# Kernel tuning notes

Measured on AMD Instinct MI355X. Metric: run time of the kernel, lower is better.

The kernel has to match this reference:

```python
import jax, jax.numpy as jnp
import numpy as np

N_NODES = 100000
N_EDGES = 1600000
N_GRAPHS = 64
D_IN, D_HID, D_OUT = 256, 128, 64
EPS = 1e-5


def gcn_conv(x, edge_index, edge_weight, W, b):
    """PyG GCNConv: add_self_loops=True, normalize=True (sym deg norm), bias."""
    n = x.shape[0]
    row = jnp.concatenate([edge_index[0], jnp.arange(n)])      # source
    col = jnp.concatenate([edge_index[1], jnp.arange(n)])      # target
    w = jnp.concatenate([edge_weight, jnp.ones((n,), x.dtype)])
    deg = jax.ops.segment_sum(w, col, num_segments=n)
    dinv = jnp.where(deg > 0, jax.lax.rsqrt(jnp.maximum(deg, EPS)), 0.0)
    norm = dinv[row] * w * dinv[col]                           # [E+N]
    h = x @ W                                                  # [N, out]
    msg = h[row] * norm[:, None]                               # [E+N, out]
    out = jax.ops.segment_sum(msg, col, num_segments=n)
    return out + b


def layer_norm(x, gamma, beta):
    mu = jnp.mean(x, axis=-1, keepdims=True)
    var = jnp.mean(jnp.square(x - mu), axis=-1, keepdims=True)
    return (x - mu) * jax.lax.rsqrt(var + EPS) * gamma + beta


def setup_inputs() -> dict:
    key = jax.random.key(0)
    ks = jax.random.split(key, 12)
    x = jax.random.normal(ks[0], (N_NODES, D_IN), jnp.float32)
    edge_index = jax.random.randint(ks[1], (2, N_EDGES), 0, N_NODES, jnp.int32)
    edge_weight = jax.random.uniform(ks[2], (N_EDGES,), jnp.float32)
    batch = jnp.sort(jax.random.randint(ks[3], (N_NODES,), 0, N_GRAPHS, jnp.int32))
    s1 = 1.0 / np.sqrt(D_IN)
    s2 = 1.0 / np.sqrt(D_HID)
    return {
        "x": x, "edge_index": edge_index, "edge_weight": edge_weight, "batch": batch,
        "W1": jax.random.uniform(ks[4], (D_IN, D_HID), jnp.float32, -s1, s1),
        "b1": jnp.zeros((D_HID,), jnp.float32),
        "g1": jnp.ones((D_HID,), jnp.float32),
        "bt1": jnp.zeros((D_HID,), jnp.float32),
        "W2": jax.random.uniform(ks[5], (D_HID, D_OUT), jnp.float32, -s2, s2),
        "b2": jnp.zeros((D_OUT,), jnp.float32),
        "g2": jnp.ones((D_OUT,), jnp.float32),
        "bt2": jnp.zeros((D_OUT,), jnp.float32),
    }


def reference(x, edge_index, edge_weight, batch, W1, b1, g1, bt1, W2, b2, g2, bt2):
    # ConvLayer 1: GCNConv -> relu -> LayerNorm(node)
    h = gcn_conv(x, edge_index, edge_weight, W1, b1)
    h = layer_norm(jax.nn.relu(h), g1, bt1)
    # dropout is identity in eval mode
    # ConvLayer 2
    h = gcn_conv(h, edge_index, edge_weight, W2, b2)
    h = layer_norm(jax.nn.relu(h), g2, bt2)
    # global mean pool over batch vector
    sums = jax.ops.segment_sum(h, batch, num_segments=N_GRAPHS)
    cnts = jax.ops.segment_sum(jnp.ones((h.shape[0],), h.dtype), batch, num_segments=N_GRAPHS)
    pooled = sums / jnp.maximum(cnts, 1.0)[:, None]
    return jax.nn.sigmoid(pooled)
```

## Files before the change

kernel.cpp:

```cpp
#include <hip/hip_runtime.h>
#include <cstdint>

#define EPSV 1e-5f

typedef __bf16 bf16x8 __attribute__((ext_vector_type(8)));
typedef __bf16 bf16x2 __attribute__((ext_vector_type(2)));
typedef float  f32x4  __attribute__((ext_vector_type(4)));
typedef unsigned long long u64;

__device__ __forceinline__ unsigned char f32_to_fp8(float x) {
    const int p = __builtin_amdgcn_cvt_pk_fp8_f32(x, x, 0, false);
    return (unsigned char)(p & 0xFF);
}

__global__ __launch_bounds__(256) void k_scanA(const u64* __restrict__ dc,
                                               float* __restrict__ dinv,
                                               int* __restrict__ cnt,
                                               int* __restrict__ bsum, int N) {
    __shared__ int ws[4];
    const int i = blockIdx.x * 256 + threadIdx.x;
    int v = 0;
    if (i < N) {
        const u64 p = dc[i];
        v = (int)(p >> 40);
        const float deg = 1.0f + (float)(p & 0xFFFFFFFFFFull) * (1.0f / 16777216.0f);
        dinv[i] = rsqrtf(deg);
        cnt[i] = v;
    }
#pragma unroll
    for (int o = 32; o >= 1; o >>= 1) v += __shfl_xor(v, o);
    if ((threadIdx.x & 63) == 0) ws[threadIdx.x >> 6] = v;
    __syncthreads();
    if (threadIdx.x == 0) bsum[blockIdx.x] = ws[0] + ws[1] + ws[2] + ws[3];
}

__global__ __launch_bounds__(256) void k_scan2(int* __restrict__ bsum, int NB) {
    __shared__ int carry;
    __shared__ int wsum[4];
    if (threadIdx.x == 0) carry = 0;
    __syncthreads();
    const int lane = threadIdx.x & 63, w = threadIdx.x >> 6;
    for (int base = 0; base < NB; base += 256) {
        const int i = base + threadIdx.x;
        const int v = (i < NB) ? bsum[i] : 0;
        int s = v;
#pragma unroll
        for (int o = 1; o < 64; o <<= 1) {
            const int t = __shfl_up(s, o);
            if (lane >= o) s += t;
        }
        if (lane == 63) wsum[w] = s;
        __syncthreads();
        int add = carry;
        for (int k = 0; k < w; ++k) add += wsum[k];
        const int tot = wsum[0] + wsum[1] + wsum[2] + wsum[3];
        if (i < NB) bsum[i] = add + s - v;
        __syncthreads();
        if (threadIdx.x == 0) carry += tot;
        __syncthreads();
    }
}

__global__ __launch_bounds__(256) void k_scan3(const int* __restrict__ cnt,
                                               const int* __restrict__ bsum,
                                               int* __restrict__ off, int N) {
    __shared__ int wsum[4];
    const int i = blockIdx.x * 256 + threadIdx.x;
    const int v = (i < N) ? cnt[i] : 0;
    const int lane = threadIdx.x & 63, w = threadIdx.x >> 6;
    int s = v;
#pragma unroll
    for (int o = 1; o < 64; o <<= 1) {
        const int t = __shfl_up(s, o);
        if (lane >= o) s += t;
    }
    if (lane == 63) wsum[w] = s;
    __syncthreads();
    int add = bsum[blockIdx.x];
    for (int k = 0; k < w; ++k) add += wsum[k];
    if (i < N) off[i] = add + s - v;
}

__global__ __launch_bounds__(256) void k_fill(const int* __restrict__ ei,
                                              const float* __restrict__ ew,
                                              const float* __restrict__ dinv,
                                              const int* __restrict__ off,
                                              const unsigned short* __restrict__ rank,
                                              float2* __restrict__ ern, int E) {
    const int e = blockIdx.x * 256 + threadIdx.x;
    if (e >= E) return;
    const int r = ei[e];
    const int c = ei[E + e];
    const int p = off[c] + (int)rank[e];
    ern[p] = make_float2(__int_as_float(r), dinv[r] * ew[e] * dinv[c]);
}

__global__ __launch_bounds__(256) void k_wcvt(const float* __restrict__ W1,
                                              __bf16* __restrict__ Wt1,
                                              const float* __restrict__ W2,
                                              __bf16* __restrict__ Wt2) {
    const int idx = blockIdx.x * 256 + threadIdx.x;
    if (idx < 256 * 128) {
        const int k = idx >> 7, c = idx & 127;
        Wt1[(((k >> 3) << 7) + c) * 8 + (k & 7)] = (__bf16)W1[idx];
    } else if (idx < 256 * 128 + 128 * 64) {
        const int j = idx - 256 * 128;
        const int k = j >> 6, c = j & 63;
        Wt2[(((k >> 3) << 6) + c) * 8 + (k & 7)] = (__bf16)W2[j];
    }
}

template <int K, int NOUT, bool ABF16>
__device__ __forceinline__ void mm_body(int bid, int tid, const void* __restrict__ Xv,
                                        const __bf16* __restrict__ WtB,
                                        unsigned char* __restrict__ H, int N) {
    constexpr int NCB = NOUT / 16;
    constexpr int NKB = K / 32;
    const int w = tid >> 6, l = tid & 63;
    const int r0 = l & 15, kq = l >> 4;
    const long tb0 = (long)bid * 128 + w * 32;
    const long ar0 = (tb0 + r0) < N ? (tb0 + r0) : (long)N - 1;
    const long ar1 = (tb0 + 16 + r0) < N ? (tb0 + 16 + r0) : (long)N - 1;

    f32x4 acc[2][NCB];
#pragma unroll
    for (int rf = 0; rf < 2; ++rf)
#pragma unroll
        for (int cb = 0; cb < NCB; ++cb) acc[rf][cb] = (f32x4){0.f, 0.f, 0.f, 0.f};

#define LDA(kb, a0, a1)                                                          \
    {                                                                            \
        const int koff = (kb) * 32 + kq * 8;                                     \
        if constexpr (ABF16) {                                                   \
            a0 = *reinterpret_cast<const bf16x8*>((const __bf16*)Xv + ar0 * K + koff); \
            a1 = *reinterpret_cast<const bf16x8*>((const __bf16*)Xv + ar1 * K + koff); \
        } else {                                                                 \
            const float* p0 = (const float*)Xv + ar0 * K + koff;                 \
            const float* p1 = (const float*)Xv + ar1 * K + koff;                 \
            const float4 u0 = *reinterpret_cast<const float4*>(p0);              \
            const float4 u1 = *reinterpret_cast<const float4*>(p0 + 4);          \
            const float4 u2 = *reinterpret_cast<const float4*>(p1);              \
            const float4 u3 = *reinterpret_cast<const float4*>(p1 + 4);          \
            a0[0] = (__bf16)u0.x; a0[1] = (__bf16)u0.y; a0[2] = (__bf16)u0.z;    \
            a0[3] = (__bf16)u0.w; a0[4] = (__bf16)u1.x; a0[5] = (__bf16)u1.y;    \
            a0[6] = (__bf16)u1.z; a0[7] = (__bf16)u1.w;                          \
            a1[0] = (__bf16)u2.x; a1[1] = (__bf16)u2.y; a1[2] = (__bf16)u2.z;    \
            a1[3] = (__bf16)u2.w; a1[4] = (__bf16)u3.x; a1[5] = (__bf16)u3.y;    \
            a1[6] = (__bf16)u3.z; a1[7] = (__bf16)u3.w;                          \
        }                                                                        \
    }

#define LDB(kb, b)                                                               \
    {                                                                            \
        const __bf16* bp = WtB + (long)(((kb) * 4 + kq) * NOUT + r0) * 8;        \
        _Pragma("unroll") for (int cb = 0; cb < NCB; ++cb)                       \
            b[cb] = *reinterpret_cast<const bf16x8*>(bp + cb * 128);             \
    }

    bf16x8 aC0, aC1, aN0, aN1;
    bf16x8 bC[NCB], bN[NCB];
    LDA(0, aC0, aC1);
    LDB(0, bC);
#pragma unroll
    for (int kb = 0; kb < NKB; ++kb) {
        if (kb + 1 < NKB) {
            LDA(kb + 1, aN0, aN1);
            LDB(kb + 1, bN);
        }
#pragma unroll
        for (int cb = 0; cb < NCB; ++cb) {
            acc[0][cb] = __builtin_amdgcn_mfma_f32_16x16x32_bf16(aC0, bC[cb], acc[0][cb], 0, 0, 0);
            acc[1][cb] = __builtin_amdgcn_mfma_f32_16x16x32_bf16(aC1, bC[cb], acc[1][cb], 0, 0, 0);
        }
        aC0 = aN0; aC1 = aN1;
#pragma unroll
        for (int cb = 0; cb < NCB; ++cb) bC[cb] = bN[cb];
    }
#undef LDA
#undef LDB

    const int orow = kq * 4;
#pragma unroll
    for (int rf = 0; rf < 2; ++rf)
#pragma unroll
        for (int cb = 0; cb < NCB; ++cb)
#pragma unroll
            for (int r = 0; r < 4; ++r) {
                const long gr = tb0 + rf * 16 + orow + r;
                if (gr < N) H[gr * NOUT + cb * 16 + r0] = f32_to_fp8(acc[rf][cb][r]);
            }
}

__global__ __launch_bounds__(256) void k_pre(const float* __restrict__ X,
                                             const __bf16* __restrict__ Wt1,
                                             unsigned char* __restrict__ H1, int N, int NBM,
                                             const int* __restrict__ ei,
                                             const float* __restrict__ ew,
                                             u64* __restrict__ dc,
                                             unsigned short* __restrict__ rank, int E) {
    if ((int)blockIdx.x < NBM) {
        mm_body<256, 128, false>(blockIdx.x, threadIdx.x, X, Wt1, H1, N);
    } else {
        const int e = ((int)blockIdx.x - NBM) * 256 + threadIdx.x;
        if (e < E) {
            const int c = ei[E + e];
            const u64 pack = (1ull << 40) | (u64)(ew[e] * 16777216.0f);
            const u64 old = atomicAdd(&dc[c], pack);
            rank[e] = (unsigned short)(old >> 40);
        }
    }
}

__global__ __launch_bounds__(256) void k_mm2(const __bf16* __restrict__ X,
                                             const __bf16* __restrict__ Wt2,
                                             unsigned char* __restrict__ H, int N) {
    mm_body<128, 64, true>(blockIdx.x, threadIdx.x, X, Wt2, H, N);
}

__global__ __launch_bounds__(256) void k_gat128(const unsigned char* __restrict__ H,
                                                const int* __restrict__ off,
                                                const int* __restrict__ cnt,
                                                const float2* __restrict__ ern,
                                                const float* __restrict__ dinv,
                                                const float* __restrict__ bias,
                                                const float* __restrict__ gm,
                                                const float* __restrict__ bt,
                                                __bf16* __restrict__ Out, int N) {
    const long wv = ((long)blockIdx.x * 256 + threadIdx.x) >> 6;
    const int lane = threadIdx.x & 63;
    if (wv >= N) return;
    const int s = off[wv];
    const int n = cnt[wv];
    const float d = dinv[wv];
    const unsigned short* Hp = reinterpret_cast<const unsigned short*>(H);

    const unsigned int h0 = Hp[wv * 64 + lane];
    float ax = __builtin_amdgcn_cvt_f32_fp8(h0, 0) * d * d;
    float ay = __builtin_amdgcn_cvt_f32_fp8(h0, 1) * d * d;

    int e = 0;
    for (; e + 8 <= n; e += 8) {
        float2 q[8];
#pragma unroll
        for (int j = 0; j < 8; ++j) q[j] = ern[s + e + j];
        unsigned int u[8];
#pragma unroll
        for (int j = 0; j < 8; ++j)
            u[j] = Hp[(long)__float_as_int(q[j].x) * 64 + lane];
#pragma unroll
        for (int j = 0; j < 8; ++j) {
            ax = fmaf(q[j].y, __builtin_amdgcn_cvt_f32_fp8(u[j], 0), ax);
            ay = fmaf(q[j].y, __builtin_amdgcn_cvt_f32_fp8(u[j], 1), ay);
        }
    }
    for (; e < n; ++e) {
        const float2 q = ern[s + e];
        const unsigned int u = Hp[(long)__float_as_int(q.x) * 64 + lane];
        ax = fmaf(q.y, __builtin_amdgcn_cvt_f32_fp8(u, 0), ax);
        ay = fmaf(q.y, __builtin_amdgcn_cvt_f32_fp8(u, 1), ay);
    }

    const float ux = fmaxf(ax + bias[2 * lane], 0.f);
    const float uy = fmaxf(ay + bias[2 * lane + 1], 0.f);
    float s1 = ux + uy, s2 = ux * ux + uy * uy;
#pragma unroll
    for (int o = 32; o >= 1; o >>= 1) {
        s1 += __shfl_xor(s1, o);
        s2 += __shfl_xor(s2, o);
    }
    const float mu = s1 * (1.f / 128.f);
    const float var = s2 * (1.f / 128.f) - mu * mu;
    const float rs = rsqrtf(var + EPSV);
    bf16x2 ob;
    ob[0] = (__bf16)((ux - mu) * rs * gm[2 * lane] + bt[2 * lane]);
    ob[1] = (__bf16)((uy - mu) * rs * gm[2 * lane + 1] + bt[2 * lane + 1]);
    reinterpret_cast<bf16x2*>(Out)[wv * 64 + lane] = ob;
}

__global__ __launch_bounds__(256) void k_gat64(const unsigned char* __restrict__ H,
                                               const int* __restrict__ off,
                                               const int* __restrict__ cnt,
                                               const float2* __restrict__ ern,
                                               const float* __restrict__ dinv,
                                               const float* __restrict__ bias,
                                               const float* __restrict__ gm,
                                               const float* __restrict__ bt,
                                               float* __restrict__ Out, int N) {
    const long wv = ((long)blockIdx.x * 256 + threadIdx.x) >> 6;
    const int lane = threadIdx.x & 63;
    if (wv >= N) return;
    const int s = off[wv];
    const int n = cnt[wv];
    const float d = dinv[wv];

    float acc = __builtin_amdgcn_cvt_f32_fp8((unsigned int)H[wv * 64 + lane], 0) * d * d;
    int e = 0;
    for (; e + 8 <= n; e += 8) {
        float2 q[8];
#pragma unroll
        for (int j = 0; j < 8; ++j) q[j] = ern[s + e + j];
        unsigned int u[8];
#pragma unroll
        for (int j = 0; j < 8; ++j)
            u[j] = H[(long)__float_as_int(q[j].x) * 64 + lane];
#pragma unroll
        for (int j = 0; j < 8; ++j)
            acc = fmaf(q[j].y, __builtin_amdgcn_cvt_f32_fp8(u[j], 0), acc);
    }
    for (; e < n; ++e) {
        const float2 q = ern[s + e];
        const unsigned int u = H[(long)__float_as_int(q.x) * 64 + lane];
        acc = fmaf(q.y, __builtin_amdgcn_cvt_f32_fp8(u, 0), acc);
    }

    const float u = fmaxf(acc + bias[lane], 0.f);
    float s1 = u, s2 = u * u;
#pragma unroll
    for (int o = 32; o >= 1; o >>= 1) {
        s1 += __shfl_xor(s1, o);
        s2 += __shfl_xor(s2, o);
    }
    const float mu = s1 * (1.f / 64.f);
    const float var = s2 * (1.f / 64.f) - mu * mu;
    const float rs = rsqrtf(var + EPSV);
    Out[wv * 64 + lane] = (u - mu) * rs * gm[lane] + bt[lane];
}

__global__ __launch_bounds__(256) void k_pool(const float* __restrict__ C,
                                              const int* __restrict__ batch,
                                              float* __restrict__ pool,
                                              int N, int chunk) {
    const int wg = blockIdx.x * 4 + (threadIdx.x >> 6);
    const int lane = threadIdx.x & 63;
    long i = (long)wg * chunk;
    const long end = (i + chunk < (long)N) ? i + chunk : (long)N;
    if (i >= end) return;

    int cur = batch[i];
    float acc = 0.f;
    int cn = 0;
    while (i < end) {
        if (i + 8 <= end && batch[i + 7] == cur) {
            float v[8];
#pragma unroll
            for (int j = 0; j < 8; ++j) v[j] = C[(i + j) * 64 + lane];
            acc += ((v[0] + v[1]) + (v[2] + v[3])) + ((v[4] + v[5]) + (v[6] + v[7]));
            cn += 8;
            i += 8;
            continue;
        }
        const int b = batch[i];
        if (b != cur) {
            unsafeAtomicAdd(&pool[cur * 64 + lane], acc);
            if (lane == 0) unsafeAtomicAdd(&pool[64 * 64 + cur], (float)cn);
            cur = b;
            acc = 0.f;
            cn = 0;
        }
        acc += C[i * 64 + lane];
        ++cn;
        ++i;
    }
    unsafeAtomicAdd(&pool[cur * 64 + lane], acc);
    if (lane == 0) unsafeAtomicAdd(&pool[64 * 64 + cur], (float)cn);
}

__global__ __launch_bounds__(256) void k_final(const float* __restrict__ pool,
                                               float* __restrict__ out) {
    const int i = blockIdx.x * 256 + threadIdx.x;
    if (i < 4096) {
        const int g = i >> 6;
        const float cnt = fmaxf(pool[64 * 64 + g], 1.0f);
        const float v = pool[i] / cnt;
        out[i] = 1.f / (1.f + expf(-v));
    }
}

extern "C" void kernel_launch(void* const* d_in, const int* in_sizes, int n_in,
                              void* d_out, int out_size, void* d_ws, size_t ws_size,
                              hipStream_t stream) {
    const float* x   = (const float*)d_in[0];
    const int*   ei  = (const int*)d_in[1];
    const float* ew  = (const float*)d_in[2];
    const int*   bat = (const int*)d_in[3];
    const float* W1  = (const float*)d_in[4];
    const float* b1  = (const float*)d_in[5];
    const float* g1  = (const float*)d_in[6];
    const float* bt1 = (const float*)d_in[7];
    const float* W2  = (const float*)d_in[8];
    const float* b2  = (const float*)d_in[9];
    const float* g2  = (const float*)d_in[10];
    const float* bt2 = (const float*)d_in[11];
    const int N = in_sizes[3];
    const int E = in_sizes[2];
    const int NB = (N + 255) / 256;

    u64*    dc   = (u64*)d_ws;
    float*  pool = (float*)(dc + N);
    float2* ern  = (float2*)(pool + 64 * 64 + 64);
    unsigned char* Ah = (unsigned char*)(ern + E);
    __bf16* Bh   = (__bf16*)(Ah + (long)N * 128);
    float*  Cf   = (float*)(Bh + (long)N * 128);
    float*  dinv = Cf + (long)N * 64;
    int*    cnt  = (int*)(dinv + N);
    int*    off  = cnt + N;
    int*    bsum = off + N;
    unsigned short* rank = (unsigned short*)(bsum + ((NB + 3) & ~3));
    __bf16* Wt1  = (__bf16*)(rank + E);
    __bf16* Wt2  = Wt1 + 128 * 256;

    const int nbE = (E + 255) / 256;
    const int nbW = (int)(((long)N * 64 + 255) / 256);
    const int NBM = (N + 127) / 128;

    hipMemsetAsync(dc, 0, (size_t)N * 8 + (64 * 64 + 64) * 4, stream);
    k_wcvt<<<(256 * 128 + 128 * 64 + 255) / 256, 256, 0, stream>>>(W1, Wt1, W2, Wt2);

    k_pre<<<NBM + nbE, 256, 0, stream>>>(x, Wt1, Ah, N, NBM, ei, ew, dc, rank, E);

    k_scanA<<<NB, 256, 0, stream>>>(dc, dinv, cnt, bsum, N);
    k_scan2<<<1, 256, 0, stream>>>(bsum, NB);
    k_scan3<<<NB, 256, 0, stream>>>(cnt, bsum, off, N);
    k_fill<<<nbE, 256, 0, stream>>>(ei, ew, dinv, off, rank, ern, E);

    k_gat128<<<nbW, 256, 0, stream>>>(Ah, off, cnt, ern, dinv, b1, g1, bt1, Bh, N);

    k_mm2<<<NBM, 256, 0, stream>>>(Bh, Wt2, Ah, N);
    k_gat64<<<nbW, 256, 0, stream>>>(Ah, off, cnt, ern, dinv, b2, g2, bt2, Cf, N);

    const int chunk = (N + 1023) / 1024;
    k_pool<<<256, 256, 0, stream>>>(Cf, bat, pool, N, chunk);
    k_final<<<16, 256, 0, stream>>>(pool, (float*)d_out);
}
```

Measured before the change: 317.9 us.

## Fuse block-sum scan into offset scan and grid-stride degree atomics ahead of GEMM

The single-block scan kernel is removed. Each block of the offset scan now sums the preceding block totals itself, which takes one launch and one serial single-block pass off the critical path at the cost of redundant reads of bsum (about 391 entries). The degree-counting part of the prologue kernel moves to a fixed set of 512 grid-stride blocks placed before the GEMM blocks, so the atomics get scheduled early and overlap with the matmul tiles. This changes the block ordering and the per-block work balance within the fused kernel.

```diff
diff --git a/kernel.cpp b/kernel.cpp
--- a/kernel.cpp
+++ b/kernel.cpp
@@ -7,6 +7,8 @@
 typedef __bf16 bf16x2 __attribute__((ext_vector_type(2)));
 typedef float  f32x4  __attribute__((ext_vector_type(4)));
 typedef unsigned long long u64;
+
+#define DEG_BLOCKS 512
 
 __device__ __forceinline__ unsigned char f32_to_fp8(float x) {
     const int p = __builtin_amdgcn_cvt_pk_fp8_f32(x, x, 0, false);
@@ -34,50 +36,35 @@
     if (threadIdx.x == 0) bsum[blockIdx.x] = ws[0] + ws[1] + ws[2] + ws[3];
 }
 
-__global__ __launch_bounds__(256) void k_scan2(int* __restrict__ bsum, int NB) {
-    __shared__ int carry;
-    __shared__ int wsum[4];
-    if (threadIdx.x == 0) carry = 0;
-    __syncthreads();
-    const int lane = threadIdx.x & 63, w = threadIdx.x >> 6;
-    for (int base = 0; base < NB; base += 256) {
-        const int i = base + threadIdx.x;
-        const int v = (i < NB) ? bsum[i] : 0;
-        int s = v;
-#pragma unroll
-        for (int o = 1; o < 64; o <<= 1) {
-            const int t = __shfl_up(s, o);
-            if (lane >= o) s += t;
-        }
-        if (lane == 63) wsum[w] = s;
-        __syncthreads();
-        int add = carry;
-        for (int k = 0; k < w; ++k) add += wsum[k];
-        const int tot = wsum[0] + wsum[1] + wsum[2] + wsum[3];
-        if (i < NB) bsum[i] = add + s - v;
-        __syncthreads();
-        if (threadIdx.x == 0) carry += tot;
-        __syncthreads();
-    }
-}
-
-__global__ __launch_bounds__(256) void k_scan3(const int* __restrict__ cnt,
+__global__ __launch_bounds__(256) void k_scanB(const int* __restrict__ cnt,
                                                const int* __restrict__ bsum,
                                                int* __restrict__ off, int N) {
-    __shared__ int wsum[4];
-    const int i = blockIdx.x * 256 + threadIdx.x;
+    __shared__ int pw[4];
+    __shared__ int lw[4];
+    __shared__ int sbase;
+    const int bid = blockIdx.x;
+    const int lane = threadIdx.x & 63, w = threadIdx.x >> 6;
+
+    int pre = 0;
+    for (int j = threadIdx.x; j < bid; j += 256) pre += bsum[j];
+#pragma unroll
+    for (int o = 32; o >= 1; o >>= 1) pre += __shfl_xor(pre, o);
+    if (lane == 0) pw[w] = pre;
+    __syncthreads();
+    if (threadIdx.x == 0) sbase = pw[0] + pw[1] + pw[2] + pw[3];
+
+    const int i = bid * 256 + threadIdx.x;
     const int v = (i < N) ? cnt[i] : 0;
-    const int lane = threadIdx.x & 63, w = threadIdx.x >> 6;
     int s = v;
 #pragma unroll
     for (int o = 1; o < 64; o <<= 1) {
         const int t = __shfl_up(s, o);
         if (lane >= o) s += t;
     }
-    if (lane == 63) wsum[w] = s;
+    if (lane == 63) lw[w] = s;
     __syncthreads();
-    int add = bsum[blockIdx.x];
-    for (int k = 0; k < w; ++k) add += wsum[k];
+    int add = sbase;
+    for (int k = 0; k < w; ++k) add += lw[k];
     if (i < N) off[i] = add + s - v;
 }
 
@@ -198,16 +185,17 @@
                                              const float* __restrict__ ew,
                                              u64* __restrict__ dc,
                                              unsigned short* __restrict__ rank, int E) {
-    if ((int)blockIdx.x < NBM) {
-        mm_body<256, 128, false>(blockIdx.x, threadIdx.x, X, Wt1, H1, N);
-    } else {
-        const int e = ((int)blockIdx.x - NBM) * 256 + threadIdx.x;
-        if (e < E) {
+    const int bid = blockIdx.x;
+    if (bid < DEG_BLOCKS) {
+        const int stride = DEG_BLOCKS * 256;
+        for (int e = bid * 256 + threadIdx.x; e < E; e += stride) {
             const int c = ei[E + e];
             const u64 pack = (1ull << 40) | (u64)(ew[e] * 16777216.0f);
             const u64 old = atomicAdd(&dc[c], pack);
             rank[e] = (unsigned short)(old >> 40);
         }
+    } else {
+        mm_body<256, 128, false>(bid - DEG_BLOCKS, threadIdx.x, X, Wt1, H1, N);
     }
 }
 
@@ -416,11 +404,10 @@
     hipMemsetAsync(dc, 0, (size_t)N * 8 + (64 * 64 + 64) * 4, stream);
     k_wcvt<<<(256 * 128 + 128 * 64 + 255) / 256, 256, 0, stream>>>(W1, Wt1, W2, Wt2);
 
-    k_pre<<<NBM + nbE, 256, 0, stream>>>(x, Wt1, Ah, N, NBM, ei, ew, dc, rank, E);
+    k_pre<<<DEG_BLOCKS + NBM, 256, 0, stream>>>(x, Wt1, Ah, N, NBM, ei, ew, dc, rank, E);
 
     k_scanA<<<NB, 256, 0, stream>>>(dc, dinv, cnt, bsum, N);
-    k_scan2<<<1, 256, 0, stream>>>(bsum, NB);
-    k_scan3<<<NB, 256, 0, stream>>>(cnt, bsum, off, N);
+    k_scanB<<<NB, 256, 0, stream>>>(cnt, bsum, off, N);
     k_fill<<<nbE, 256, 0, stream>>>(ei, ew, dinv, off, rank, ern, E);
 
     k_gat128<<<nbW, 256, 0, stream>>>(Ah, off, cnt, ern, dinv, b1, g1, bt1, Bh, N);
```

After: 314.5 us. Within noise of the previous version (-1.0%).
